# Optimization experiments

Hardware: AMD Instinct MI355X
Metric: run time of the kernel (lower is better)

The kernel has to match this reference:

```python
import jax, jax.numpy as jnp
from jax import lax
import numpy as np

EPS_START, EPS_END, EPS_DECAY = 1.0, 0.05, 10000.0


def gru_step(x, h, w_ih, w_hh, b_ih, b_hh):
    # PyTorch GRUCell math; gates stacked as [r, z, n]
    gi = x @ w_ih.T + b_ih
    gh = h @ w_hh.T + b_hh
    i_r, i_z, i_n = jnp.split(gi, 3, axis=1)
    h_r, h_z, h_n = jnp.split(gh, 3, axis=1)
    r = jax.nn.sigmoid(i_r + h_r)
    z = jax.nn.sigmoid(i_z + h_z)
    n = jnp.tanh(i_n + r * h_n)
    return (1.0 - z) * n + z * h


def setup_inputs() -> dict:
    key = jax.random.key(0)
    ks = jax.random.split(key, 7)
    V, E, H = 32000, 256, 512
    s = 0.05
    return {
        "embedding": jax.random.normal(ks[0], (V, E), jnp.float32) * s,
        "w_ih": jax.random.normal(ks[1], (3 * H, E), jnp.float32) * s,
        "w_hh": jax.random.normal(ks[2], (3 * H, H), jnp.float32) * s,
        "b_ih": jax.random.normal(ks[3], (3 * H,), jnp.float32) * s,
        "b_hh": jax.random.normal(ks[4], (3 * H,), jnp.float32) * s,
        "w_out": jax.random.normal(ks[5], (V, H), jnp.float32) * s,
        "b_out": jax.random.normal(ks[6], (V,), jnp.float32) * s,
        "seq_len": 256,
        "batch_size": 512,
    }


def reference(embedding, w_ih, w_hh, b_ih, b_hh, w_out, b_out, seq_len, batch_size):
    V, E = embedding.shape
    H = w_hh.shape[1]
    B = batch_size
    log_unif = jnp.float32(np.log(V))  # -log(vocab_size) fill for epsilon-greedy

    keys = jax.random.split(jax.random.key(42), seq_len)
    ts = jnp.arange(seq_len, dtype=jnp.float32)

    h0 = jnp.zeros((B, H), jnp.float32)
    x0 = jnp.broadcast_to(embedding[0], (B, E))  # start token id 0

    def step(carry, inp):
        h, x = carry
        t, k = inp
        k_eps, k_gum = jax.random.split(k)
        h = gru_step(x, h, w_ih, w_hh, b_ih, b_hh)
        logp = jax.nn.log_softmax(h @ w_out.T + b_out, axis=1)  # [B, V]
        eps_t = EPS_END + (EPS_START - EPS_END) * jnp.exp(-4.0 * t / EPS_DECAY)
        draw = eps_t >= jax.random.uniform(k_eps, (B,))
        masked = jnp.where(draw[:, None], -log_unif, logp)
        g = jax.random.gumbel(k_gum, (B, V), jnp.float32)
        sampled = jnp.argmax(masked + g, axis=1)  # [B] int
        lp = jnp.take_along_axis(logp, sampled[:, None], axis=1)[:, 0]
        x_next = embedding[sampled]
        return (h, x_next), (sampled, lp)

    _, (samples, lps) = lax.scan(step, (h0, x0), (ts, keys))
    return samples.T, lps.T  # [B, S] each
```

## Files before the change

### kernel.cpp

```cpp
#include <hip/hip_runtime.h>
#include <math.h>
#include <stdio.h>

#ifndef JAX_PARTITIONABLE
#define JAX_PARTITIONABLE 1
#endif

namespace {

constexpr int B  = 512;
constexpr int S  = 256;
constexpr int E  = 256;
constexpr int H  = 512;
constexpr int V  = 32000;
constexpr int G3 = 3 * H;
constexpr int VBLK = 64;
constexpr int NCH  = V / VBLK;
constexpr int NDMAX = 96;

typedef __bf16 bf16x8 __attribute__((ext_vector_type(8)));
typedef float  f32x4  __attribute__((ext_vector_type(4)));
typedef unsigned u32x4 __attribute__((ext_vector_type(4)));

__device__ __forceinline__ void tf2x32(unsigned k0, unsigned k1,
                                       unsigned x0, unsigned x1,
                                       unsigned& o0, unsigned& o1) {
  unsigned ks2 = k0 ^ k1 ^ 0x1BD11BDAu;
  x0 += k0; x1 += k1;
#define TFR(r) { x0 += x1; x1 = (x1 << (r)) | (x1 >> (32 - (r))); x1 ^= x0; }
  TFR(13) TFR(15) TFR(26) TFR(6)   x0 += k1;  x1 += ks2 + 1u;
  TFR(17) TFR(29) TFR(16) TFR(24)  x0 += ks2; x1 += k0 + 2u;
  TFR(13) TFR(15) TFR(26) TFR(6)   x0 += k0;  x1 += k1 + 3u;
  TFR(17) TFR(29) TFR(16) TFR(24)  x0 += k1;  x1 += ks2 + 4u;
  TFR(13) TFR(15) TFR(26) TFR(6)   x0 += ks2; x1 += k0 + 5u;
#undef TFR
  o0 = x0; o1 = x1;
}

__device__ __forceinline__ unsigned rbits(unsigned g0, unsigned g1,
                                          unsigned b, unsigned v) {
#if JAX_PARTITIONABLE
  unsigned y0, y1;
  tf2x32(g0, g1, 0u, b * (unsigned)V + v, y0, y1);
  return y0 ^ y1;
#else
  const unsigned N2 = (unsigned)(B/2) * (unsigned)V;
  unsigned ii = b * (unsigned)V + v;
  unsigned jj = (b < 256) ? ii : ii - N2;
  unsigned y0, y1;
  tf2x32(g0, g1, jj, N2 + jj, y0, y1);
  return (b < 256) ? y0 : y1;
#endif
}

__device__ __forceinline__ float u01_from_bits(unsigned bits) {
  return __uint_as_float(0x3f800000u | (bits >> 9)) - 1.0f;
}

__device__ __forceinline__ float gumbel_exact(unsigned bits) {
  float u = u01_from_bits(bits);
  if (u == 0.0f) u = 1.1754943508222875e-38f;
  float w = (float)(-log((double)u));
  return (float)(-log((double)w));
}

__device__ __forceinline__ float gumbel_fast(unsigned bits) {
  float u = u01_from_bits(bits);
  if (u == 0.0f) u = 1.1754943508222875e-38f;
  float w = -__logf(u);
  return -__logf(w);
}

__device__ __forceinline__ unsigned short f2bf(float f) {
  unsigned u = __float_as_uint(f);
  unsigned r = (u + 0x7fffu + ((u >> 16) & 1u)) >> 16;
  return (unsigned short)r;
}

__device__ __forceinline__ size_t frag_off(int row, int k, int kTiles) {
  return ((size_t)((row >> 4) * kTiles + (k >> 5)) * 64
          + (row & 15) + 16 * ((k >> 3) & 3)) * 8 + (k & 7);
}

__global__ void k_init_rng(unsigned* __restrict__ kq, unsigned* __restrict__ ke) {
  int t = threadIdx.x;
  unsigned h0, h1, e0, e1, g0, g1;
#if JAX_PARTITIONABLE
  tf2x32(0u, 42u, 0u, (unsigned)t, h0, h1);
  tf2x32(h0, h1, 0u, 0u, e0, e1);
  tf2x32(h0, h1, 0u, 1u, g0, g1);
#else
  unsigned a0, a1, b0, b1;
  if (t < 128) {
    tf2x32(0u, 42u, (unsigned)(2*t),   (unsigned)(256+2*t), a0, a1);
    tf2x32(0u, 42u, (unsigned)(2*t+1), (unsigned)(257+2*t), b0, b1);
    h0 = a0; h1 = b0;
  } else {
    int j = 2*t - 256;
    tf2x32(0u, 42u, (unsigned)j,     (unsigned)(256+j), a0, a1);
    tf2x32(0u, 42u, (unsigned)(j+1), (unsigned)(257+j), b0, b1);
    h0 = a1; h1 = b1;
  }
  unsigned p0, p1, q0, q1;
  tf2x32(h0, h1, 0u, 2u, p0, p1);
  tf2x32(h0, h1, 1u, 3u, q0, q1);
  e0 = p0; e1 = q0; g0 = p1; g1 = q1;
#endif
  ke[2*t] = e0; ke[2*t+1] = e1;
  kq[2*t] = g0; kq[2*t+1] = g1;
}

__global__ void k_init_draws(const unsigned* __restrict__ ke,
                             unsigned char* __restrict__ draws) {
  int t = blockIdx.x;
  int b = threadIdx.x;
  unsigned k0 = ke[2*t], k1 = ke[2*t+1];
  unsigned bits, y0, y1;
#if JAX_PARTITIONABLE
  tf2x32(k0, k1, 0u, (unsigned)b, y0, y1);
  bits = y0 ^ y1;
#else
  if (b < 256) { tf2x32(k0, k1, (unsigned)b,       (unsigned)(256+b), y0, y1); bits = y0; }
  else         { tf2x32(k0, k1, (unsigned)(b-256), (unsigned)b,       y0, y1); bits = y1; }
#endif
  float u   = u01_from_bits(bits);
  float tf  = (float)t;
  float ex  = expf(__fmul_rn(-4.0f, tf) / 10000.0f);
  float eps = __fadd_rn(0.05f, __fmul_rn(0.95f, ex));
  draws[t*B + b] = (eps >= u) ? 1 : 0;
}

__global__ void k_init_nd(const unsigned char* __restrict__ draws,
                          int* __restrict__ nd_slot) {
  int t = blockIdx.x;
  if (threadIdx.x != 0) return;
  int cnt = 0;
  for (int b = 0; b < B; b++) {
    if (!draws[t*B + b] && cnt < NDMAX) nd_slot[t*B + b] = cnt++;
    else nd_slot[t*B + b] = -1;
  }
}

__global__ __launch_bounds__(256) void k_pre_argmax(
    const unsigned* __restrict__ kq, const unsigned char* __restrict__ draws,
    int* __restrict__ pre) {
  const int job  = blockIdx.x * 4 + (threadIdx.x >> 6);
  const int lane = threadIdx.x & 63;
  const int t = job >> 9, b = job & (B - 1);
  if (!draws[t*B + b]) { if (lane == 0) pre[job] = -1; return; }
  const unsigned g0 = kq[2*t], g1 = kq[2*t+1];
  unsigned best = 0u; int bv = V;
  for (int v = lane; v < V; v += 64) {
    unsigned bits = rbits(g0, g1, (unsigned)b, (unsigned)v) >> 9;
    if (bits > best || (bits == best && v < bv)) { best = bits; bv = v; }
  }
#pragma unroll
  for (int m = 1; m < 64; m <<= 1) {
    unsigned ob = __shfl_xor(best, m, 64);
    int      ov = __shfl_xor(bv,   m, 64);
    if (ob > best || (ob == best && ov < bv)) { best = ob; bv = ov; }
  }
  if (lane == 0) pre[job] = bv;
}

__global__ void k_init_state(float* __restrict__ h, int* __restrict__ samp) {
  int b = blockIdx.x, tid = threadIdx.x;
  h[b*H + tid] = 0.0f;
  h[b*H + 256 + tid] = 0.0f;
  if (tid == 0) samp[b] = 0;
}

__global__ void k_cast_w(const float* __restrict__ w,
                         unsigned short* __restrict__ w_sw) {
  int g = blockIdx.x*256 + threadIdx.x;
  int v  = g >> 6;
  int k0 = (g & 63) * 8;
  const float* src = w + (size_t)v*H + k0;
  union { unsigned short s[8]; u32x4 vv; } u;
#pragma unroll
  for (int e = 0; e < 8; e++) u.s[e] = f2bf(src[e]);
  *(u32x4*)&w_sw[frag_off(v, k0, H/32)] = u.vv;
}

__device__ __forceinline__ float sigm_acc(float v) {
  return (float)(1.0 / (1.0 + exp(-(double)v)));
}
__device__ __forceinline__ float tanh_acc(float v) {
  return (float)tanh((double)v);
}

__global__ __launch_bounds__(256) void k_gates_finish(
    const float* __restrict__ h, const float* __restrict__ w_hh,
    const float* __restrict__ b_hh, float* __restrict__ gh,
    const float* __restrict__ pmax, const float* __restrict__ psum,
    const float* __restrict__ plog,
    const int* __restrict__ pre, const int* __restrict__ nd_slot,
    const float* __restrict__ nd_keys, const float* __restrict__ nd_kmax,
    const unsigned* __restrict__ kq,
    const float* __restrict__ w_out, const float* __restrict__ b_out,
    float* __restrict__ out_samples, float* __restrict__ out_lps,
    int* __restrict__ samp, int t) {
  const int tid = threadIdx.x;
  union Sh {
    struct { float As[2][16][68]; float Ws[2][16][52]; } g;
    struct { float sA[256]; int cand[160]; float ck[160]; float cl[160];
             int ccnt; int samp; float blog; } f;
  };
  __shared__ Sh sh;

  if (blockIdx.x < 256) {
    if (t >= S) return;
    const int jw = tid & 15, rg = tid >> 4;
    const int j0 = (blockIdx.x & 31) * 16;
    const int row0 = (blockIdx.x >> 5) * 64;
    float ah[4][3] = {};
    float pa[4], pw[3];
#pragma unroll
    for (int l = 0; l < 4; l++) {
      int idx = tid + l*256;
      pa[l] = h[(size_t)(row0 + (idx >> 4))*H + (idx & 15)];
    }
#pragma unroll
    for (int l = 0; l < 3; l++) {
      int idx = tid + l*256;
      int c = idx >> 4;
      pw[l] = w_hh[(size_t)((c >> 4)*512 + j0 + (c & 15))*H + (idx & 15)];
    }
#pragma unroll
    for (int l = 0; l < 4; l++) {
      int idx = tid + l*256;
      sh.g.As[0][idx & 15][idx >> 4] = pa[l];
    }
#pragma unroll
    for (int l = 0; l < 3; l++) {
      int idx = tid + l*256;
      sh.g.Ws[0][idx & 15][idx >> 4] = pw[l];
    }
    __syncthreads();
    int p = 0;
#pragma unroll 1
    for (int tile = 0; tile < 32; tile++) {
      if (tile < 31) {
        const int k0 = (tile + 1) * 16;
#pragma unroll
        for (int l = 0; l < 4; l++) {
          int idx = tid + l*256;
          pa[l] = h[(size_t)(row0 + (idx >> 4))*H + k0 + (idx & 15)];
        }
#pragma unroll
        for (int l = 0; l < 3; l++) {
          int idx = tid + l*256;
          int c = idx >> 4;
          pw[l] = w_hh[(size_t)((c >> 4)*512 + j0 + (c & 15))*H + k0 + (idx & 15)];
        }
      }
#pragma unroll
      for (int kk = 0; kk < 16; kk++) {
        const float4 av = *(const float4*)&sh.g.As[p][kk][rg*4];
        const float a[4] = {av.x, av.y, av.z, av.w};
        const float w0 = sh.g.Ws[p][kk][jw];
        const float w1 = sh.g.Ws[p][kk][16 + jw];
        const float w2 = sh.g.Ws[p][kk][32 + jw];
#pragma unroll
        for (int i = 0; i < 4; i++) {
          ah[i][0] = fmaf(a[i], w0, ah[i][0]);
          ah[i][1] = fmaf(a[i], w1, ah[i][1]);
          ah[i][2] = fmaf(a[i], w2, ah[i][2]);
        }
      }
      if (tile < 31) {
#pragma unroll
        for (int l = 0; l < 4; l++) {
          int idx = tid + l*256;
          sh.g.As[p ^ 1][idx & 15][idx >> 4] = pa[l];
        }
#pragma unroll
        for (int l = 0; l < 3; l++) {
          int idx = tid + l*256;
          sh.g.Ws[p ^ 1][idx & 15][idx >> 4] = pw[l];
        }
        __syncthreads();
        p ^= 1;
      }
    }
    const int j = j0 + jw;
    const float bh_r = b_hh[j], bh_z = b_hh[512 + j], bh_n = b_hh[1024 + j];
#pragma unroll
    for (int i = 0; i < 4; i++) {
      const int b = row0 + rg*4 + i;
      gh[(size_t)b*G3 +        j] = __fadd_rn(ah[i][0], bh_r);
      gh[(size_t)b*G3 +  512 + j] = __fadd_rn(ah[i][1], bh_z);
      gh[(size_t)b*G3 + 1024 + j] = __fadd_rn(ah[i][2], bh_n);
    }
    return;
  }

  const int tf = t - 1;
  if (tf < 0) return;
  const int b = blockIdx.x - 256;
  const int* pre_t     = pre + tf*B;
  const int* nd_slot_t = nd_slot + tf*B;

  float m = -INFINITY;
  for (int c = tid; c < NCH; c += 256) m = fmaxf(m, pmax[b*NCH + c]);
  sh.f.sA[tid] = m; __syncthreads();
  for (int s = 128; s > 0; s >>= 1) {
    if (tid < s) sh.f.sA[tid] = fmaxf(sh.f.sA[tid], sh.f.sA[tid+s]);
    __syncthreads();
  }
  const float M = sh.f.sA[0];
  __syncthreads();
  float sum = 0.0f;
  for (int c = tid; c < NCH; c += 256)
    sum += psum[b*NCH + c] * expf(pmax[b*NCH + c] - M);
  sh.f.sA[tid] = sum; __syncthreads();
  for (int s = 128; s > 0; s >>= 1) {
    if (tid < s) sh.f.sA[tid] += sh.f.sA[tid+s];
    __syncthreads();
  }
  const float SUM = sh.f.sA[0];
  __syncthreads();

  const int pr = pre_t[b];
  if (pr >= 0) {
    if (tid == 0) { sh.f.samp = pr; sh.f.blog = plog[b]; }
  } else {
    const int slot = nd_slot_t[b];
    if (slot < 0) {
      if (tid == 0) { sh.f.samp = 0; sh.f.blog = plog[b]; }
    } else {
      const unsigned g0 = kq[2*tf], g1 = kq[2*tf+1];
      if (tid == 0) sh.f.ccnt = 0;
      float km = -INFINITY;
      for (int c = tid; c < NCH; c += 256) km = fmaxf(km, nd_kmax[slot*NCH + c]);
      sh.f.sA[tid] = km; __syncthreads();
      for (int s = 128; s > 0; s >>= 1) {
        if (tid < s) sh.f.sA[tid] = fmaxf(sh.f.sA[tid], sh.f.sA[tid+s]);
        __syncthreads();
      }
      const float thr = sh.f.sA[0] - 0.0859375f;
      __syncthreads();
      const float* keys = nd_keys + (size_t)slot*V;
      for (int c = tid; c < NCH; c += 256) {
        if (nd_kmax[slot*NCH + c] >= thr) {
          for (int j = 0; j < VBLK; j++) {
            float k = keys[c*VBLK + j];
            if (k >= thr) {
              int p = atomicAdd(&sh.f.ccnt, 1);
              if (p < 160) sh.f.cand[p] = c*VBLK + j;
            }
          }
        }
      }
      __syncthreads();
      const int nc = min(sh.f.ccnt, 160);
      const int wid = tid >> 6, lane = tid & 63;
      for (int c = wid; c < nc; c += 4) {
        const int v = sh.f.cand[c];
        const float* wr = w_out + (size_t)v*H;
        const float* hr = h + (size_t)b*H;
        float s = 0.0f;
#pragma unroll
        for (int i = 0; i < 8; i++) s = fmaf(hr[lane + 64*i], wr[lane + 64*i], s);
#pragma unroll
        for (int mm = 1; mm < 64; mm <<= 1) s += __shfl_xor(s, mm, 64);
        if (lane == 0) {
          float logit = __fadd_rn(s, b_out[v]);
          float key   = __fadd_rn(logit,
                          gumbel_exact(rbits(g0, g1, (unsigned)b, (unsigned)v)));
          sh.f.ck[c] = key; sh.f.cl[c] = logit;
        }
      }
      __syncthreads();
      if (tid == 0) {
        float bk = -INFINITY; int bv = V; float bl = 0.0f;
        for (int c = 0; c < nc; c++) {
          float k = sh.f.ck[c]; int v = sh.f.cand[c];
          if (k > bk || (k == bk && v < bv)) { bk = k; bv = v; bl = sh.f.cl[c]; }
        }
        sh.f.samp = bv; sh.f.blog = bl;
      }
    }
  }
  __syncthreads();
  if (tid == 0) {
    const int sampled = sh.f.samp;
    float lse = (float)log((double)SUM);
    float lp  = __fsub_rn(__fsub_rn(sh.f.blog, M), lse);
    out_samples[b*S + tf] = (float)sampled;
    out_lps[b*S + tf]     = lp;
    samp[b] = sampled;
  }
}

__global__ __launch_bounds__(256) void k_xgru(
    const float* __restrict__ emb, const int* __restrict__ samp,
    const float* __restrict__ w_ih, const float* __restrict__ b_ih,
    const float* __restrict__ gh, float* __restrict__ h,
    unsigned short* __restrict__ h_sw) {
  __shared__ __align__(16) float As[2][16][68];
  __shared__ __align__(16) float Ws[2][16][52];
  __shared__ int srow[64];
  const int tid = threadIdx.x;
  const int jw = tid & 15, rg = tid >> 4;
  const int j0 = blockIdx.x * 16;
  const int row0 = blockIdx.y * 64;
  if (tid < 64) srow[tid] = samp[row0 + tid];
  __syncthreads();

  float ai[4][3] = {};
  float pa[4], pw[3];
#pragma unroll
  for (int l = 0; l < 4; l++) {
    int idx = tid + l*256;
    pa[l] = emb[(size_t)srow[idx >> 4]*E + (idx & 15)];
  }
#pragma unroll
  for (int l = 0; l < 3; l++) {
    int idx = tid + l*256;
    int c = idx >> 4;
    pw[l] = w_ih[(size_t)((c >> 4)*512 + j0 + (c & 15))*E + (idx & 15)];
  }
#pragma unroll
  for (int l = 0; l < 4; l++) {
    int idx = tid + l*256;
    As[0][idx & 15][idx >> 4] = pa[l];
  }
#pragma unroll
  for (int l = 0; l < 3; l++) {
    int idx = tid + l*256;
    Ws[0][idx & 15][idx >> 4] = pw[l];
  }
  __syncthreads();
  int p = 0;
#pragma unroll 1
  for (int tile = 0; tile < 16; tile++) {
    if (tile < 15) {
      const int k0 = (tile + 1) * 16;
#pragma unroll
      for (int l = 0; l < 4; l++) {
        int idx = tid + l*256;
        pa[l] = emb[(size_t)srow[idx >> 4]*E + k0 + (idx & 15)];
      }
#pragma unroll
      for (int l = 0; l < 3; l++) {
        int idx = tid + l*256;
        int c = idx >> 4;
        pw[l] = w_ih[(size_t)((c >> 4)*512 + j0 + (c & 15))*E + k0 + (idx & 15)];
      }
    }
#pragma unroll
    for (int kk = 0; kk < 16; kk++) {
      const float4 av = *(const float4*)&As[p][kk][rg*4];
      const float a[4] = {av.x, av.y, av.z, av.w};
      const float w0 = Ws[p][kk][jw];
      const float w1 = Ws[p][kk][16 + jw];
      const float w2 = Ws[p][kk][32 + jw];
#pragma unroll
      for (int i = 0; i < 4; i++) {
        ai[i][0] = fmaf(a[i], w0, ai[i][0]);
        ai[i][1] = fmaf(a[i], w1, ai[i][1]);
        ai[i][2] = fmaf(a[i], w2, ai[i][2]);
      }
    }
    if (tile < 15) {
#pragma unroll
      for (int l = 0; l < 4; l++) {
        int idx = tid + l*256;
        As[p ^ 1][idx & 15][idx >> 4] = pa[l];
      }
#pragma unroll
      for (int l = 0; l < 3; l++) {
        int idx = tid + l*256;
        Ws[p ^ 1][idx & 15][idx >> 4] = pw[l];
      }
      __syncthreads();
      p ^= 1;
    }
  }

  const int j = j0 + jw;
  const float bi_r = b_ih[j], bi_z = b_ih[512 + j], bi_n = b_ih[1024 + j];
#pragma unroll
  for (int i = 0; i < 4; i++) {
    const int b = row0 + rg*4 + i;
    float gi_r = __fadd_rn(ai[i][0], bi_r);
    float gi_z = __fadd_rn(ai[i][1], bi_z);
    float gi_n = __fadd_rn(ai[i][2], bi_n);
    float gh_r = gh[(size_t)b*G3 + j];
    float gh_z = gh[(size_t)b*G3 + 512 + j];
    float gh_n = gh[(size_t)b*G3 + 1024 + j];
    float r  = sigm_acc(__fadd_rn(gi_r, gh_r));
    float zz = sigm_acc(__fadd_rn(gi_z, gh_z));
    float nn = tanh_acc(__fadd_rn(gi_n, __fmul_rn(r, gh_n)));
    float hv = h[(size_t)b*H + j];
    float t1 = __fmul_rn(__fsub_rn(1.0f, zz), nn);
    float t2 = __fmul_rn(zz, hv);
    float hn = __fadd_rn(t1, t2);
    h[(size_t)b*H + j] = hn;
    h_sw[frag_off(b, j, H/32)] = f2bf(hn);
  }
}

__global__ __launch_bounds__(256) void k_mfma_logits(
    const unsigned short* __restrict__ h_sw,
    const unsigned short* __restrict__ w_sw,
    const float* __restrict__ b_out,
    const unsigned* __restrict__ kq,
    const unsigned char* __restrict__ draws,
    int* __restrict__ pre,
    const int* __restrict__ nd_slot_t,
    float* __restrict__ pmax, float* __restrict__ psum,
    float* __restrict__ plog,
    float* __restrict__ nd_keys, float* __restrict__ nd_kmax, int t) {
  const int tid  = threadIdx.x;

  if (blockIdx.y == 0) {
    __shared__ unsigned sb[4];
    __shared__ int      sv[4];
    const int tn = t + 1;
    if (tn >= S) return;
    const int b = blockIdx.x;
    if (!draws[tn*B + b]) { if (tid == 0) pre[tn*B + b] = -1; return; }
    const unsigned g0 = kq[2*tn], g1 = kq[2*tn+1];
    unsigned best = 0u; int bv = V;
    for (int v = tid; v < V; v += 256) {
      unsigned bits = rbits(g0, g1, (unsigned)b, (unsigned)v) >> 9;
      if (bits > best || (bits == best && v < bv)) { best = bits; bv = v; }
    }
#pragma unroll
    for (int m = 1; m < 64; m <<= 1) {
      unsigned ob = __shfl_xor(best, m, 64);
      int      ov = __shfl_xor(bv,   m, 64);
      if (ob > best || (ob == best && ov < bv)) { best = ob; bv = ov; }
    }
    const int wv = tid >> 6;
    if ((tid & 63) == 0) { sb[wv] = best; sv[wv] = bv; }
    __syncthreads();
    if (tid == 0) {
      for (int i = 1; i < 4; i++) {
        unsigned ob = sb[i]; int ov = sv[i];
        if (ob > best || (ob == best && ov < bv)) { best = ob; bv = ov; }
      }
      pre[tn*B + b] = bv;
    }
    return;
  }

  const int L  = (blockIdx.y - 1) * 512 + blockIdx.x;
  const int wg = (L & 7) * 128 + (L >> 3);
  if (wg >= 2*NCH) return;
  const int vblk = wg >> 1;
  const int bblk = wg & 1;
  const int* __restrict__ pre_t = pre + t*B;
  const int lane = tid & 63, w = tid >> 6;
  const int quad = lane >> 4, l15 = lane & 15;

  f32x4 acc[4][4] = {};

  const int mtBase = bblk*16 + w*4;
  const int ntBase = vblk*4;
  const unsigned short* hp = h_sw + (size_t)mtBase*16*512 + lane*8;
  const unsigned short* wp = w_sw + (size_t)ntBase*16*512 + lane*8;

  bf16x8 afc[4], bfc[4];
#pragma unroll
  for (int mt = 0; mt < 4; mt++)
    afc[mt] = __builtin_bit_cast(bf16x8, *(const u32x4*)(hp + (size_t)(mt*16)*512));
#pragma unroll
  for (int nt = 0; nt < 4; nt++)
    bfc[nt] = __builtin_bit_cast(bf16x8, *(const u32x4*)(wp + (size_t)(nt*16)*512));

#pragma unroll 1
  for (int kt = 0; kt < 15; kt++) {
    bf16x8 afn[4], bfn[4];
#pragma unroll
    for (int mt = 0; mt < 4; mt++)
      afn[mt] = __builtin_bit_cast(bf16x8,
          *(const u32x4*)(hp + (size_t)(mt*16 + kt + 1)*512));
#pragma unroll
    for (int nt = 0; nt < 4; nt++)
      bfn[nt] = __builtin_bit_cast(bf16x8,
          *(const u32x4*)(wp + (size_t)(nt*16 + kt + 1)*512));
#pragma unroll
    for (int mt = 0; mt < 4; mt++)
#pragma unroll
      for (int nt = 0; nt < 4; nt++)
        acc[mt][nt] = __builtin_amdgcn_mfma_f32_16x16x32_bf16(
            afc[mt], bfc[nt], acc[mt][nt], 0, 0, 0);
#pragma unroll
    for (int mt = 0; mt < 4; mt++) afc[mt] = afn[mt];
#pragma unroll
    for (int nt = 0; nt < 4; nt++) bfc[nt] = bfn[nt];
  }
  {
#pragma unroll
    for (int mt = 0; mt < 4; mt++)
#pragma unroll
      for (int nt = 0; nt < 4; nt++)
        acc[mt][nt] = __builtin_amdgcn_mfma_f32_16x16x32_bf16(
            afc[mt], bfc[nt], acc[mt][nt], 0, 0, 0);
  }

  const int bW = bblk*256 + w*64;
  const int vW = vblk*64;
  const unsigned g0 = kq[2*t], g1 = kq[2*t+1];
  float bias[4];
#pragma unroll
  for (int nt = 0; nt < 4; nt++) bias[nt] = b_out[vW + nt*16 + l15];

#pragma unroll
  for (int mt = 0; mt < 4; mt++) {
#pragma unroll
    for (int r = 0; r < 4; r++) {
      const int b = bW + mt*16 + quad*4 + r;
      float lg[4];
#pragma unroll
      for (int nt = 0; nt < 4; nt++) lg[nt] = acc[mt][nt][r] + bias[nt];
      float lmax = fmaxf(fmaxf(lg[0], lg[1]), fmaxf(lg[2], lg[3]));
#pragma unroll
      for (int m = 1; m < 16; m <<= 1) lmax = fmaxf(lmax, __shfl_xor(lmax, m, 64));
      float ls = 0.0f;
#pragma unroll
      for (int nt = 0; nt < 4; nt++) ls += __expf(lg[nt] - lmax);
#pragma unroll
      for (int m = 1; m < 16; m <<= 1) ls += __shfl_xor(ls, m, 64);
      if (l15 == 0) { pmax[b*NCH + vblk] = lmax; psum[b*NCH + vblk] = ls; }
      const int pr = pre_t[b];
      if (pr >= 0) {
        int rel = pr - vW;
        if (rel >= 0 && rel < 64 && (rel & 15) == l15) plog[b] = lg[rel >> 4];
      } else {
        const int slot = nd_slot_t[b];
        if (slot >= 0) {
          float key[4];
#pragma unroll
          for (int nt = 0; nt < 4; nt++)
            key[nt] = lg[nt] + gumbel_fast(
                rbits(g0, g1, (unsigned)b, (unsigned)(vW + nt*16 + l15)));
          float* dst = nd_keys + (size_t)slot*V + vW + l15;
#pragma unroll
          for (int nt = 0; nt < 4; nt++) dst[nt*16] = key[nt];
          float kmx = fmaxf(fmaxf(key[0], key[1]), fmaxf(key[2], key[3]));
#pragma unroll
          for (int m = 1; m < 16; m <<= 1) kmx = fmaxf(kmx, __shfl_xor(kmx, m, 64));
          if (l15 == 0) nd_kmax[slot*NCH + vblk] = kmx;
        }
      }
    }
  }
}

}

extern "C" void kernel_launch(void* const* d_in, const int* in_sizes, int n_in,
                              void* d_out, int out_size, void* d_ws, size_t ws_size,
                              hipStream_t stream) {
  (void)in_sizes; (void)n_in; (void)out_size;
  const float* emb   = (const float*)d_in[0];
  const float* w_ih  = (const float*)d_in[1];
  const float* w_hh  = (const float*)d_in[2];
  const float* b_ih  = (const float*)d_in[3];
  const float* b_hh  = (const float*)d_in[4];
  const float* w_out = (const float*)d_in[5];
  const float* b_out = (const float*)d_in[6];
  float* out = (float*)d_out;

  char* wsb = (char*)d_ws;
  size_t off = 0;
  auto alloc = [&](size_t nbytes) {
    char* p = wsb + off;
    off += (nbytes + 255) & ~size_t(255);
    return p;
  };
  float* h     = (float*)alloc((size_t)B*H*4);
  float* gh    = (float*)alloc((size_t)B*G3*4);
  unsigned short* h_sw = (unsigned short*)alloc((size_t)B*H*2);
  unsigned short* w_sw = (unsigned short*)alloc((size_t)V*H*2);
  float* pmax  = (float*)alloc((size_t)B*NCH*4);
  float* psum  = (float*)alloc((size_t)B*NCH*4);
  float* plog  = (float*)alloc((size_t)B*4);
  unsigned* kq = (unsigned*)alloc((size_t)S*2*4);
  unsigned* ke = (unsigned*)alloc((size_t)S*2*4);
  unsigned char* draws = (unsigned char*)alloc((size_t)S*B);
  int* pre     = (int*)alloc((size_t)S*B*4);
  int* nd_slot = (int*)alloc((size_t)S*B*4);
  float* nd_keys = (float*)alloc((size_t)NDMAX*V*4);
  float* nd_kmax = (float*)alloc((size_t)NDMAX*NCH*4);
  int* samp    = (int*)alloc((size_t)B*4);
  if (off > ws_size) {
    fprintf(stderr, "kernel_launch: workspace too small (need %zu, have %zu)\n",
            off, ws_size);
    return;
  }

  k_init_rng<<<1, S, 0, stream>>>(kq, ke);
  k_init_draws<<<S, B, 0, stream>>>(ke, draws);
  k_init_nd<<<S, 64, 0, stream>>>(draws, nd_slot);
  k_pre_argmax<<<B/4, 256, 0, stream>>>(kq, draws, pre);
  k_init_state<<<B, 256, 0, stream>>>(h, samp);
  k_cast_w<<<(V*H/8)/256, 256, 0, stream>>>(w_out, w_sw);

  for (int t = 0; t < S; t++) {
    k_gates_finish<<<768, 256, 0, stream>>>(
        h, w_hh, b_hh, gh, pmax, psum, plog, pre, nd_slot,
        nd_keys, nd_kmax, kq, w_out, b_out,
        out, out + (size_t)B*S, samp, t);
    k_xgru<<<dim3(32, 8), 256, 0, stream>>>(emb, samp, w_ih, b_ih,
                                            gh, h, h_sw);
    k_mfma_logits<<<dim3(512, 3), 256, 0, stream>>>(
        h_sw, w_sw, b_out, kq, draws, pre, nd_slot + t*B,
        pmax, psum, plog, nd_keys, nd_kmax, t);
  }
  k_gates_finish<<<768, 256, 0, stream>>>(
      h, w_hh, b_hh, gh, pmax, psum, plog, pre, nd_slot,
      nd_keys, nd_kmax, kq, w_out, b_out,
      out, out + (size_t)B*S, samp, S);
}
```

Measured before the change: 34.70 ms.

## Precompute embedding input-gate table and move pre-argmax blocks into gates kernel

Computes emb @ w_ih^T + b_ih for the whole vocabulary once (a V x 3H table), so each step's input-gate GEMM turns into a row gather by sampled token inside a simple elementwise GRU kernel. The per-step epsilon pre-argmax blocks move from the logits kernel into the gates/finish kernel launch, which shrinks the logits grid. This needs about 196 MB of workspace and falls back to the old path when that space is missing. The one-time table GEMM runs in plain fp32 FMA and costs extra setup time.

```diff
diff --git a/kernel.cpp b/kernel.cpp
--- a/kernel.cpp
+++ b/kernel.cpp
@@ -182,6 +182,50 @@
   *(u32x4*)&w_sw[frag_off(v, k0, H/32)] = u.vv;
 }
 
+__global__ __launch_bounds__(512) void k_emb_gates(
+    const float* __restrict__ emb, const float* __restrict__ w_ih,
+    const float* __restrict__ b_ih, float* __restrict__ EG) {
+  __shared__ __align__(16) float As[16][68];
+  __shared__ __align__(16) float Ws[16][68];
+  const int tid = threadIdx.x;
+  const int tx = tid & 15, ty = tid >> 4;
+  const int row0 = blockIdx.y * 64, col0 = blockIdx.x * 64;
+  float acc[2][4] = {};
+  for (int k0 = 0; k0 < E; k0 += 16) {
+#pragma unroll
+    for (int l = 0; l < 2; l++) {
+      int idx = tid + l*512;
+      int r = idx >> 4, kk = idx & 15;
+      As[kk][r] = emb[(size_t)(row0 + r)*E + k0 + kk];
+      Ws[kk][r] = w_ih[(size_t)(col0 + r)*E + k0 + kk];
+    }
+    __syncthreads();
+#pragma unroll
+    for (int kk = 0; kk < 16; kk++) {
+      const float2 av = *(const float2*)&As[kk][ty*2];
+      const float4 wv = *(const float4*)&Ws[kk][tx*4];
+      const float a[2] = {av.x, av.y};
+      const float w[4] = {wv.x, wv.y, wv.z, wv.w};
+#pragma unroll
+      for (int i = 0; i < 2; i++)
+#pragma unroll
+        for (int j = 0; j < 4; j++) acc[i][j] = fmaf(a[i], w[j], acc[i][j]);
+    }
+    __syncthreads();
+  }
+#pragma unroll
+  for (int i = 0; i < 2; i++) {
+    int r = row0 + ty*2 + i;
+    int c = col0 + tx*4;
+    float4 o;
+    o.x = __fadd_rn(acc[i][0], b_ih[c + 0]);
+    o.y = __fadd_rn(acc[i][1], b_ih[c + 1]);
+    o.z = __fadd_rn(acc[i][2], b_ih[c + 2]);
+    o.w = __fadd_rn(acc[i][3], b_ih[c + 3]);
+    *(float4*)&EG[(size_t)r*G3 + c] = o;
+  }
+}
+
 __device__ __forceinline__ float sigm_acc(float v) {
   return (float)(1.0 / (1.0 + exp(-(double)v)));
 }
@@ -194,9 +238,9 @@
     const float* __restrict__ b_hh, float* __restrict__ gh,
     const float* __restrict__ pmax, const float* __restrict__ psum,
     const float* __restrict__ plog,
-    const int* __restrict__ pre, const int* __restrict__ nd_slot,
+    int* __restrict__ pre, const int* __restrict__ nd_slot,
     const float* __restrict__ nd_keys, const float* __restrict__ nd_kmax,
-    const unsigned* __restrict__ kq,
+    const unsigned* __restrict__ kq, const unsigned char* __restrict__ draws,
     const float* __restrict__ w_out, const float* __restrict__ b_out,
     float* __restrict__ out_samples, float* __restrict__ out_lps,
     int* __restrict__ samp, int t) {
@@ -205,6 +249,7 @@
     struct { float As[2][16][68]; float Ws[2][16][52]; } g;
     struct { float sA[256]; int cand[160]; float ck[160]; float cl[160];
              int ccnt; int samp; float blog; } f;
+    struct { unsigned sb[4]; int sv[4]; } p;
   };
   __shared__ Sh sh;
 
@@ -291,6 +336,36 @@
       gh[(size_t)b*G3 +        j] = __fadd_rn(ah[i][0], bh_r);
       gh[(size_t)b*G3 +  512 + j] = __fadd_rn(ah[i][1], bh_z);
       gh[(size_t)b*G3 + 1024 + j] = __fadd_rn(ah[i][2], bh_n);
+    }
+    return;
+  }
+
+  if (blockIdx.x >= 768) {
+    const int tn = t + 1;
+    if (tn >= S) return;
+    const int b = blockIdx.x - 768;
+    if (!draws[tn*B + b]) { if (tid == 0) pre[tn*B + b] = -1; return; }
+    const unsigned g0 = kq[2*tn], g1 = kq[2*tn+1];
+    unsigned best = 0u; int bv = V;
+    for (int v = tid; v < V; v += 256) {
+      unsigned bits = rbits(g0, g1, (unsigned)b, (unsigned)v) >> 9;
+      if (bits > best || (bits == best && v < bv)) { best = bits; bv = v; }
+    }
+#pragma unroll
+    for (int m = 1; m < 64; m <<= 1) {
+      unsigned ob = __shfl_xor(best, m, 64);
+      int      ov = __shfl_xor(bv,   m, 64);
+      if (ob > best || (ob == best && ov < bv)) { best = ob; bv = ov; }
+    }
+    const int wv = tid >> 6;
+    if ((tid & 63) == 0) { sh.p.sb[wv] = best; sh.p.sv[wv] = bv; }
+    __syncthreads();
+    if (tid == 0) {
+      for (int i = 1; i < 4; i++) {
+        unsigned ob = sh.p.sb[i]; int ov = sh.p.sv[i];
+        if (ob > best || (ob == best && ov < bv)) { best = ob; bv = ov; }
+      }
+      pre[tn*B + b] = bv;
     }
     return;
   }
@@ -391,6 +466,33 @@
     out_lps[b*S + tf]     = lp;
     samp[b] = sampled;
   }
+}
+
+__global__ void k_gru(const float* __restrict__ EG, const int* __restrict__ samp,
+                      const float* __restrict__ gh, float* __restrict__ h,
+                      unsigned short* __restrict__ h_sw) {
+  int g = blockIdx.x*256 + threadIdx.x;
+  int b  = g >> 6;
+  int j0 = (g & 63) * 8;
+  const float* gib = EG + (size_t)samp[b]*G3;
+  const float* ghb = gh + (size_t)b*G3;
+  float hn[8];
+  union { unsigned short s[8]; u32x4 vv; } u;
+#pragma unroll
+  for (int e = 0; e < 8; e++) {
+    int j = j0 + e;
+    float r  = sigm_acc(__fadd_rn(gib[j],     ghb[j]));
+    float zz = sigm_acc(__fadd_rn(gib[H+j],   ghb[H+j]));
+    float nn = tanh_acc(__fadd_rn(gib[2*H+j], __fmul_rn(r, ghb[2*H+j])));
+    float hv = h[(size_t)b*H + j];
+    float t1 = __fmul_rn(__fsub_rn(1.0f, zz), nn);
+    float t2 = __fmul_rn(zz, hv);
+    hn[e] = __fadd_rn(t1, t2);
+    u.s[e] = f2bf(hn[e]);
+  }
+#pragma unroll
+  for (int e = 0; e < 8; e++) h[(size_t)b*H + j0 + e] = hn[e];
+  *(u32x4*)&h_sw[frag_off(b, j0, H/32)] = u.vv;
 }
 
 __global__ __launch_bounds__(256) void k_xgru(
@@ -507,52 +609,18 @@
     const unsigned short* __restrict__ w_sw,
     const float* __restrict__ b_out,
     const unsigned* __restrict__ kq,
-    const unsigned char* __restrict__ draws,
-    int* __restrict__ pre,
+    const int* __restrict__ pre_t,
     const int* __restrict__ nd_slot_t,
     float* __restrict__ pmax, float* __restrict__ psum,
     float* __restrict__ plog,
     float* __restrict__ nd_keys, float* __restrict__ nd_kmax, int t) {
   const int tid  = threadIdx.x;
 
-  if (blockIdx.y == 0) {
-    __shared__ unsigned sb[4];
-    __shared__ int      sv[4];
-    const int tn = t + 1;
-    if (tn >= S) return;
-    const int b = blockIdx.x;
-    if (!draws[tn*B + b]) { if (tid == 0) pre[tn*B + b] = -1; return; }
-    const unsigned g0 = kq[2*tn], g1 = kq[2*tn+1];
-    unsigned best = 0u; int bv = V;
-    for (int v = tid; v < V; v += 256) {
-      unsigned bits = rbits(g0, g1, (unsigned)b, (unsigned)v) >> 9;
-      if (bits > best || (bits == best && v < bv)) { best = bits; bv = v; }
-    }
-#pragma unroll
-    for (int m = 1; m < 64; m <<= 1) {
-      unsigned ob = __shfl_xor(best, m, 64);
-      int      ov = __shfl_xor(bv,   m, 64);
-      if (ob > best || (ob == best && ov < bv)) { best = ob; bv = ov; }
-    }
-    const int wv = tid >> 6;
-    if ((tid & 63) == 0) { sb[wv] = best; sv[wv] = bv; }
-    __syncthreads();
-    if (tid == 0) {
-      for (int i = 1; i < 4; i++) {
-        unsigned ob = sb[i]; int ov = sv[i];
-        if (ob > best || (ob == best && ov < bv)) { best = ob; bv = ov; }
-      }
-      pre[tn*B + b] = bv;
-    }
-    return;
-  }
-
-  const int L  = (blockIdx.y - 1) * 512 + blockIdx.x;
+  const int L  = blockIdx.y * 512 + blockIdx.x;
   const int wg = (L & 7) * 128 + (L >> 3);
   if (wg >= 2*NCH) return;
   const int vblk = wg >> 1;
   const int bblk = wg & 1;
-  const int* __restrict__ pre_t = pre + t*B;
   const int lane = tid & 63, w = tid >> 6;
   const int quad = lane >> 4, l15 = lane & 15;
 
@@ -693,6 +761,9 @@
             off, ws_size);
     return;
   }
+  const size_t eg_bytes = ((size_t)V*G3*4 + 255) & ~size_t(255);
+  const bool use_eg = (off + eg_bytes <= ws_size);
+  float* EG = use_eg ? (float*)alloc(eg_bytes) : nullptr;
 
   k_init_rng<<<1, S, 0, stream>>>(kq, ke);
   k_init_draws<<<S, B, 0, stream>>>(ke, draws);
@@ -700,20 +771,25 @@
   k_pre_argmax<<<B/4, 256, 0, stream>>>(kq, draws, pre);
   k_init_state<<<B, 256, 0, stream>>>(h, samp);
   k_cast_w<<<(V*H/8)/256, 256, 0, stream>>>(w_out, w_sw);
+  if (use_eg)
+    k_emb_gates<<<dim3(G3/64, V/64), 512, 0, stream>>>(emb, w_ih, b_ih, EG);
 
   for (int t = 0; t < S; t++) {
-    k_gates_finish<<<768, 256, 0, stream>>>(
+    k_gates_finish<<<1280, 256, 0, stream>>>(
         h, w_hh, b_hh, gh, pmax, psum, plog, pre, nd_slot,
-        nd_keys, nd_kmax, kq, w_out, b_out,
+        nd_keys, nd_kmax, kq, draws, w_out, b_out,
         out, out + (size_t)B*S, samp, t);
-    k_xgru<<<dim3(32, 8), 256, 0, stream>>>(emb, samp, w_ih, b_ih,
-                                            gh, h, h_sw);
-    k_mfma_logits<<<dim3(512, 3), 256, 0, stream>>>(
-        h_sw, w_sw, b_out, kq, draws, pre, nd_slot + t*B,
+    if (use_eg)
+      k_gru<<<(B*H/8)/256, 256, 0, stream>>>(EG, samp, gh, h, h_sw);
+    else
+      k_xgru<<<dim3(32, 8), 256, 0, stream>>>(emb, samp, w_ih, b_ih,
+                                              gh, h, h_sw);
+    k_mfma_logits<<<dim3(512, 2), 256, 0, stream>>>(
+        h_sw, w_sw, b_out, kq, pre + t*B, nd_slot + t*B,
         pmax, psum, plog, nd_keys, nd_kmax, t);
   }
-  k_gates_finish<<<768, 256, 0, stream>>>(
+  k_gates_finish<<<1280, 256, 0, stream>>>(
       h, w_hh, b_hh, gh, pmax, psum, plog, pre, nd_slot,
-      nd_keys, nd_kmax, kq, w_out, b_out,
+      nd_keys, nd_kmax, kq, draws, w_out, b_out,
       out, out + (size_t)B*S, samp, S);
 }
```

Result: faster. 33.87 ms (-2.4%).
